# Kernel optimization log

Hardware: AMD Instinct MI355X
Metric: run time of the kernel (lower is better)

The kernel has to match this reference:

```python
import jax, jax.numpy as jnp
import numpy as np

NEG_SLOPE = 0.2  # PyG GATConv default
BN_EPS = 1e-5
NUM_GRAPHS = 128


def _bn(x, g, b, m, v):
    # eval-mode BatchNorm1d with running stats
    return (x - m) * jax.lax.rsqrt(v + BN_EPS) * g + b


def _gat_conv(x, src, dst, mask, W, a_src, a_dst, bias):
    # PyG GATConv: per-head linear, edge logits LeakyReLU(a_src.Wx_j + a_dst.Wx_i),
    # segment-softmax over incoming edges of each dst node, scatter-add messages.
    N = x.shape[0]
    H, C = a_src.shape
    xw = (x @ W).reshape(N, H, C)                       # [N,H,C]
    logit_s = (xw * a_src).sum(-1)                      # [N,H]
    logit_d = (xw * a_dst).sum(-1)                      # [N,H]
    e = jax.nn.leaky_relu(logit_s[src] + logit_d[dst], NEG_SLOPE)  # [E,H]
    e = jnp.where(mask[:, None], e, -1e30)              # edges filtered by edge_weights==1
    m = jax.ops.segment_max(e, dst, num_segments=N)     # [N,H]
    m = jnp.maximum(m, -1e30)                           # guard empty segments
    p = jnp.exp(e - m[dst]) * mask[:, None].astype(e.dtype)
    denom = jax.ops.segment_sum(p, dst, num_segments=N) + 1e-16
    alpha = p / denom[dst]                              # [E,H]
    out = jax.ops.segment_sum(xw[src] * alpha[..., None], dst, num_segments=N)
    return out.reshape(N, H * C) + bias


def setup_inputs() -> dict:
    key = jax.random.key(0)
    ks = jax.random.split(key, 20)
    N, E, F, G, NC = 20000, 320000, 128, NUM_GRAPHS, 10
    E0, E1, H = 256, 512, 2
    C = E1 // H

    def lin(k, fi, fo):
        return jax.random.normal(k, (fi, fo), jnp.float32) / np.float32(np.sqrt(fi))

    def bn(k, n):
        k1, k2, k3, k4 = jax.random.split(k, 4)
        g = 1.0 + 0.1 * jax.random.normal(k1, (n,), jnp.float32)
        b = 0.1 * jax.random.normal(k2, (n,), jnp.float32)
        m = 0.1 * jax.random.normal(k3, (n,), jnp.float32)
        v = 1.0 + 0.5 * jax.random.uniform(k4, (n,), jnp.float32)
        return g, b, m, v

    d = {}
    d['x'] = jax.random.normal(ks[0], (N, F), jnp.float32)
    d['edge_index'] = jax.random.randint(ks[1], (2, E), 0, N, dtype=jnp.int32)
    d['edge_weights'] = jnp.ones((E,), jnp.int32)
    d['batch'] = jnp.sort(jax.random.randint(ks[2], (N,), 0, G, dtype=jnp.int32))
    d['mlp_w1'] = lin(ks[3], F, E0); d['mlp_b1'] = jnp.zeros((E0,), jnp.float32)
    d['bn1_g'], d['bn1_b'], d['bn1_m'], d['bn1_v'] = bn(ks[4], E0)
    d['mlp_w2'] = lin(ks[5], E0, E0); d['mlp_b2'] = jnp.zeros((E0,), jnp.float32)
    d['bn2_g'], d['bn2_b'], d['bn2_m'], d['bn2_v'] = bn(ks[6], E0)
    d['gat0_w'] = lin(ks[7], E0, H * C)
    d['gat0_asrc'] = 0.1 * jax.random.normal(ks[8], (H, C), jnp.float32)
    d['gat0_adst'] = 0.1 * jax.random.normal(ks[9], (H, C), jnp.float32)
    d['gat0_bias'] = jnp.zeros((H * C,), jnp.float32)
    d['gat1_w'] = lin(ks[10], E1, H * C)
    d['gat1_asrc'] = 0.1 * jax.random.normal(ks[11], (H, C), jnp.float32)
    d['gat1_adst'] = 0.1 * jax.random.normal(ks[12], (H, C), jnp.float32)
    d['gat1_bias'] = jnp.zeros((H * C,), jnp.float32)
    d['bn3_g'], d['bn3_b'], d['bn3_m'], d['bn3_v'] = bn(ks[13], E1)
    d['fin_w1'] = lin(ks[14], E1, E1); d['fin_b1'] = jnp.zeros((E1,), jnp.float32)
    d['fin_w2'] = lin(ks[15], E1, NC); d['fin_b2'] = jnp.zeros((NC,), jnp.float32)
    return d


def reference(x, edge_index, edge_weights, batch,
              mlp_w1, mlp_b1, bn1_g, bn1_b, bn1_m, bn1_v,
              mlp_w2, mlp_b2, bn2_g, bn2_b, bn2_m, bn2_v,
              gat0_w, gat0_asrc, gat0_adst, gat0_bias,
              gat1_w, gat1_asrc, gat1_adst, gat1_bias,
              bn3_g, bn3_b, bn3_m, bn3_v,
              fin_w1, fin_b1, fin_w2, fin_b2):
    src, dst = edge_index[0], edge_index[1]
    mask = edge_weights == 1
    # initial MLP (dropout is identity in eval)
    h = jax.nn.relu(_bn(x @ mlp_w1 + mlp_b1, bn1_g, bn1_b, bn1_m, bn1_v))
    h = jax.nn.relu(_bn(h @ mlp_w2 + mlp_b2, bn2_g, bn2_b, bn2_m, bn2_v))
    # GAT layers
    h = _gat_conv(h, src, dst, mask, gat0_w, gat0_asrc, gat0_adst, gat0_bias)
    h = _gat_conv(h, src, dst, mask, gat1_w, gat1_asrc, gat1_adst, gat1_bias)
    # global mean pool over graphs
    sums = jax.ops.segment_sum(h, batch, num_segments=NUM_GRAPHS)
    cnt = jax.ops.segment_sum(jnp.ones((h.shape[0], 1), h.dtype), batch, num_segments=NUM_GRAPHS)
    pooled = sums / jnp.maximum(cnt, 1.0)
    # final head: BN -> ReLU -> Linear -> ReLU -> Linear
    z = jax.nn.relu(_bn(pooled, bn3_g, bn3_b, bn3_m, bn3_v))
    z = jax.nn.relu(z @ fin_w1 + fin_b1)
    return z @ fin_w2 + fin_b2
```

## Files before the change

kernel.cpp:

```cpp
#include <hip/hip_runtime.h>

typedef unsigned short u16;

constexpr int NN = 20000;
constexpr int EE = 320000;
constexpr int FD = 128;
constexpr int C0 = 256;
constexpr int C1 = 512;
constexpr int NG = 128;
constexpr int NC = 10;
constexpr int NBLK = (NN + 255) / 256;
constexpr int HB  = 320;
constexpr int EST = HB * 256;

constexpr size_t OFF_XB   = 0;
constexpr size_t OFF_H1   = OFF_XB  + (size_t)NN * FD * 2;
constexpr size_t OFF_H2   = OFF_H1  + (size_t)NN * C0 * 2;
constexpr size_t OFF_XW   = OFF_H2  + (size_t)NN * C0 * 2;
constexpr size_t OFF_H34  = OFF_XW  + (size_t)NN * C1 * 2;
constexpr size_t OFF_LS   = OFF_H34 + (size_t)NN * C1 * 2;
constexpr size_t OFF_LD   = OFF_LS  + (size_t)NN * 2 * 4;
constexpr size_t OFF_DEG  = OFF_LD  + (size_t)NN * 2 * 4;
constexpr size_t OFF_OFFS = OFF_DEG + (size_t)NN * 4;
constexpr size_t OFF_CUR  = OFF_OFFS + 80016;
constexpr size_t OFF_CSRC = OFF_CUR + (size_t)NN * 4;
constexpr size_t OFF_GCNT = OFF_CSRC + (size_t)EE * 4;
constexpr size_t OFF_GOFF = OFF_GCNT + 512;
constexpr size_t OFF_PART = OFF_GOFF + 768;
constexpr size_t OFF_PTOT = OFF_PART + 512;
constexpr size_t OFF_Z1   = OFF_PTOT + 256;
constexpr size_t OFF_Z2   = OFF_Z1  + (size_t)NG * C1 * 2;
constexpr size_t OFF_ST   = OFF_Z2  + (size_t)NG * C1 * 2;
constexpr size_t OFF_W1T  = OFF_ST  + 8192;
constexpr size_t OFF_W2T  = OFF_W1T + (size_t)FD * C0 * 2;
constexpr size_t OFF_G0T  = OFF_W2T + (size_t)C0 * C0 * 2;
constexpr size_t OFF_G1T  = OFF_G0T + (size_t)C0 * C1 * 2;
constexpr size_t OFF_AUX  = OFF_G1T + (size_t)C1 * C1 * 2;
constexpr size_t OFF_FLAG = OFF_AUX  + 0;
constexpr size_t OFF_A0S  = OFF_AUX  + 256;
constexpr size_t OFF_A0D  = OFF_AUX  + 1280;
constexpr size_t OFF_A1S  = OFF_AUX  + 2304;
constexpr size_t OFF_A1D  = OFF_AUX  + 3328;
constexpr size_t OFF_GB0  = OFF_AUX  + 4352;
constexpr size_t OFF_GB1  = OFF_AUX  + 6400;
constexpr size_t OFF_FB1  = OFF_AUX  + 8448;
constexpr size_t OFF_FB2  = OFF_AUX  + 10496;
constexpr size_t OFF_GMX  = OFF_AUX  + 10752;

__device__ inline float bf2f(u16 u) { return __uint_as_float(((unsigned)u) << 16); }
__device__ inline u16 f2bf(float f) {
    unsigned u = __float_as_uint(f);
    unsigned r = u + 0x7fffu + ((u >> 16) & 1u);
    return (u16)(r >> 16);
}
__device__ inline float ldf(const void* p, long i, unsigned f) {
    return f ? ((const float*)p)[i] : bf2f(((const u16*)p)[i]);
}
__device__ inline unsigned encf(float f) {
    unsigned u = __float_as_uint(f);
    return (u & 0x80000000u) ? ~u : (u | 0x80000000u);
}
__device__ inline float decf(unsigned e) {
    return (e & 0x80000000u) ? __uint_as_float(e ^ 0x80000000u) : __uint_as_float(~e);
}
__device__ inline void unpack8(uint4 r, float* v) {
    v[0] = bf2f((u16)(r.x & 0xffff)); v[1] = bf2f((u16)(r.x >> 16));
    v[2] = bf2f((u16)(r.y & 0xffff)); v[3] = bf2f((u16)(r.y >> 16));
    v[4] = bf2f((u16)(r.z & 0xffff)); v[5] = bf2f((u16)(r.z >> 16));
    v[6] = bf2f((u16)(r.w & 0xffff)); v[7] = bf2f((u16)(r.w >> 16));
}

typedef __bf16 bf16x8_t __attribute__((ext_vector_type(8)));
typedef float  f32x4_t  __attribute__((ext_vector_type(4)));

__device__ __forceinline__ void gl_lds16(const u16* g, u16* l) {
    __builtin_amdgcn_global_load_lds((const __attribute__((address_space(1))) void*)g,
                                     (__attribute__((address_space(3))) void*)l, 16, 0, 0);
}

__global__ void detect_dtype(const u16* __restrict__ x, const u16* __restrict__ w,
                             const u16* __restrict__ fw, unsigned* flag) {
    __shared__ int cnt;
    if (threadIdx.x == 0) cnt = 0;
    __syncthreads();
    int c = 0;
    for (int i = threadIdx.x; i < 4096; i += 256) {
        c += (((x[i]  >> 7) & 0xFF) == 0xFF);
        c += (((w[i]  >> 7) & 0xFF) == 0xFF);
        c += (((fw[i] >> 7) & 0xFF) == 0xFF);
    }
    atomicAdd(&cnt, c);
    __syncthreads();
    if (threadIdx.x == 0) *flag = (cnt >= 2) ? 1u : 0u;
}

__global__ void cvt_x(const unsigned* __restrict__ flag, const void* __restrict__ xin,
                      u16* __restrict__ XB, int* __restrict__ deg, int* __restrict__ gcnt,
                      unsigned* __restrict__ gmxu) {
    int i = blockIdx.x * 256 + threadIdx.x;
    if (i < NN) deg[i] = 0;
    if (i < NG) gcnt[i] = 0;
    if (i < 4)  gmxu[i] = encf(-1e30f);
    if (*flag) {
        float4 v = ((const float4*)xin)[i];
        ushort4 r;
        r.x = f2bf(v.x); r.y = f2bf(v.y); r.z = f2bf(v.z); r.w = f2bf(v.w);
        ((ushort4*)XB)[i] = r;
    } else {
        ((ushort4*)XB)[i] = ((const ushort4*)xin)[i];
    }
}

__global__ void prep_params(const unsigned* __restrict__ flag,
                            const void* g1, const void* b1, const void* m1, const void* v1, const void* lb1,
                            const void* g2, const void* b2, const void* m2, const void* v2, const void* lb2,
                            const void* g3, const void* b3, const void* m3, const void* v3,
                            const void* a0s, const void* a0d, const void* gb0in,
                            const void* a1s, const void* a1d, const void* gb1in,
                            const void* fb1in, const void* fb2in,
                            float* S1, float* T1, float* S2, float* T2, float* S3, float* T3,
                            u16* A0S, u16* A0D, u16* A1S, u16* A1D,
                            float* GB0, float* GB1, float* FB1, float* FB2) {
    unsigned f = *flag;
    int c = threadIdx.x;
    if (c < 256) {
        float s = ldf(g1, c, f) / sqrtf(ldf(v1, c, f) + 1e-5f);
        S1[c] = s; T1[c] = s * (ldf(lb1, c, f) - ldf(m1, c, f)) + ldf(b1, c, f);
        float s2 = ldf(g2, c, f) / sqrtf(ldf(v2, c, f) + 1e-5f);
        S2[c] = s2; T2[c] = s2 * (ldf(lb2, c, f) - ldf(m2, c, f)) + ldf(b2, c, f);
    }
    float s3 = ldf(g3, c, f) / sqrtf(ldf(v3, c, f) + 1e-5f);
    S3[c] = s3; T3[c] = ldf(b3, c, f) - ldf(m3, c, f) * s3;
    A0S[c] = f2bf(ldf(a0s, c, f));
    A0D[c] = f2bf(ldf(a0d, c, f));
    A1S[c] = f2bf(ldf(a1s, c, f));
    A1D[c] = f2bf(ldf(a1d, c, f));
    GB0[c] = ldf(gb0in, c, f);
    GB1[c] = ldf(gb1in, c, f);
    FB1[c] = ldf(fb1in, c, f);
    if (c < NC) FB2[c] = ldf(fb2in, c, f);
}

__global__ void transpose_all(const unsigned* __restrict__ flag,
                              const void* __restrict__ w1, const void* __restrict__ w2,
                              const void* __restrict__ g0, const void* __restrict__ g1,
                              u16* __restrict__ w1T, u16* __restrict__ w2T,
                              u16* __restrict__ g0T, u16* __restrict__ g1T) {
    int b = blockIdx.x;
    const void* B; u16* BT; int K, logN, base;
    if (b < 128)      { B = w1; BT = w1T; K = FD; logN = 8; base = 0; }
    else if (b < 384) { B = w2; BT = w2T; K = C0; logN = 8; base = 128; }
    else if (b < 896) { B = g0; BT = g0T; K = C0; logN = 9; base = 384; }
    else              { B = g1; BT = g1T; K = C1; logN = 9; base = 896; }
    int idx = (b - base) * 256 + threadIdx.x;
    int N = 1 << logN;
    int k = idx >> logN, n = idx & (N - 1);
    u16 v = (*flag) ? f2bf(((const float*)B)[idx]) : ((const u16*)B)[idx];
    BT[(size_t)n * K + k] = v;
}

__global__ __launch_bounds__(256) void hist_k(const int* __restrict__ dst, const int* __restrict__ ew,
                                              const int* __restrict__ batch,
                                              int* __restrict__ deg, int* __restrict__ gcnt) {
    int tid = blockIdx.x * 256 + threadIdx.x;
    int lane = threadIdx.x & 63;
#pragma unroll
    for (int j = 0; j < 4; j++) {
        int e = tid + j * EST;
        if (e < EE && ew[e] == 1) atomicAdd(&deg[dst[e]], 1);
    }
    int n = tid;
    if (n < NN) {
        int g = batch[n];
        int pg = __shfl_up(g, 1);
        bool head = (lane == 0) || (pg != g);
        unsigned long long act = __ballot(1);
        unsigned long long hm  = __ballot(head);
        if (head) {
            unsigned long long above = (lane < 63) ? ((hm >> (lane + 1)) << (lane + 1)) : 0ull;
            int limit = 64 - __builtin_clzll(act);
            int nxt = above ? __builtin_ctzll(above) : limit;
            atomicAdd(&gcnt[g], nxt - lane);
        }
    }
}
__global__ __launch_bounds__(256) void scan_blk(const int* __restrict__ deg, int* __restrict__ off,
                                                int* __restrict__ part) {
    __shared__ int tmp[256];
    int tid = threadIdx.x, i = blockIdx.x * 256 + tid;
    int v = (i < NN) ? deg[i] : 0;
    tmp[tid] = v;
    __syncthreads();
#pragma unroll
    for (int s = 1; s < 256; s <<= 1) {
        int a = (tid >= s) ? tmp[tid - s] : 0;
        __syncthreads();
        if (tid >= s) tmp[tid] += a;
        __syncthreads();
    }
    if (i < NN) off[i] = tmp[tid] - v;
    if (tid == 255) part[blockIdx.x] = tmp[255];
}
__global__ __launch_bounds__(128) void scan_small(int* __restrict__ part, int* __restrict__ ptot,
                                                  const int* __restrict__ gcnt, int* __restrict__ goff) {
    __shared__ int tmp[128];
    int tid = threadIdx.x;
    int v = (tid < NBLK) ? part[tid] : 0;
    tmp[tid] = v;
    __syncthreads();
#pragma unroll
    for (int s = 1; s < 128; s <<= 1) {
        int a = (tid >= s) ? tmp[tid - s] : 0;
        __syncthreads();
        if (tid >= s) tmp[tid] += a;
        __syncthreads();
    }
    if (tid < NBLK) part[tid] = tmp[tid] - v;
    if (tid == 127) *ptot = tmp[127];
    __syncthreads();
    int g = gcnt[tid];
    tmp[tid] = g;
    __syncthreads();
#pragma unroll
    for (int s = 1; s < 128; s <<= 1) {
        int a = (tid >= s) ? tmp[tid - s] : 0;
        __syncthreads();
        if (tid >= s) tmp[tid] += a;
        __syncthreads();
    }
    goff[tid] = tmp[tid] - g;
    if (tid == 127) goff[128] = tmp[127];
}
__global__ __launch_bounds__(256) void scan_add(int* __restrict__ off, const int* __restrict__ part,
                                                const int* __restrict__ ptot, int* __restrict__ cursor) {
    int tid = threadIdx.x, i = blockIdx.x * 256 + tid;
    if (i < NN) {
        int o = off[i] + part[blockIdx.x];
        off[i] = o;
        cursor[i] = o;
    }
    if (i == 0) off[NN] = *ptot;
}
__global__ __launch_bounds__(256) void csr_fill(const int* __restrict__ src, const int* __restrict__ dst,
                                                const int* __restrict__ ew,
                                                int* __restrict__ cursor, int* __restrict__ csrc) {
    int tid = blockIdx.x * 256 + threadIdx.x;
    bool ok[4]; int sv[4]; int p[4];
#pragma unroll
    for (int j = 0; j < 4; j++) {
        int e = tid + j * EST;
        ok[j] = false; sv[j] = 0; p[j] = 0;
        if (e < EE && ew[e] == 1) {
            ok[j] = true;
            sv[j] = src[e];
            p[j] = atomicAdd(&cursor[dst[e]], 1);
        }
    }
#pragma unroll
    for (int j = 0; j < 4; j++) if (ok[j]) csrc[p[j]] = sv[j];
}

template <int EPI>
__global__ __launch_bounds__(256) void gemm_tile(const u16* __restrict__ A, const u16* __restrict__ BT,
                                                 u16* __restrict__ Cm,
                                                 const float* __restrict__ S, const float* __restrict__ T,
                                                 int M, int N, int K) {
    __shared__ u16 As[64 * 32];
    __shared__ u16 Bs[128 * 32];
    const int tid  = threadIdx.x;
    const int wave = tid >> 6;
    const int lane = tid & 63;
    const int quad = lane >> 4;
    const int l16  = lane & 15;
    const int wr0  = (wave >> 1) * 32;
    const int wc0  = (wave & 1) * 64;
    const int row0 = blockIdx.x * 64;
    const int col0 = blockIdx.y * 128;

    const int lr = lane >> 2;
    const int lk = (lane & 3) * 8;
    const u16* gp[3];
    u16* lp[3];
#pragma unroll
    for (int j = 0; j < 3; j++) {
        int t = wave * 3 + j;
        if (t < 4) {
            int rl = t * 16 + lr;
            int gr = row0 + rl; if (gr >= M) gr = M - 1;
            gp[j] = A + (size_t)gr * K + lk;
            lp[j] = As + t * 512 + lane * 8;
        } else {
            int bl = (t - 4) * 16 + lr;
            gp[j] = BT + (size_t)(col0 + bl) * K + lk;
            lp[j] = Bs + (t - 4) * 512 + lane * 8;
        }
    }

    f32x4_t acc[2][4];
#pragma unroll
    for (int r = 0; r < 2; r++)
#pragma unroll
        for (int c = 0; c < 4; c++)
#pragma unroll
            for (int i = 0; i < 4; i++) acc[r][c][i] = 0.f;

    for (int k0 = 0; k0 < K; k0 += 32) {
#pragma unroll
        for (int j = 0; j < 3; j++) gl_lds16(gp[j] + k0, lp[j]);
        __syncthreads();

        bf16x8_t a[2], b[4];
#pragma unroll
        for (int r = 0; r < 2; r++)
            a[r] = *(const bf16x8_t*)(As + (size_t)(wr0 + r * 16 + l16) * 32 + quad * 8);
#pragma unroll
        for (int c = 0; c < 4; c++)
            b[c] = *(const bf16x8_t*)(Bs + (size_t)(wc0 + c * 16 + l16) * 32 + quad * 8);
#pragma unroll
        for (int r = 0; r < 2; r++)
#pragma unroll
            for (int c = 0; c < 4; c++)
                acc[r][c] = __builtin_amdgcn_mfma_f32_16x16x32_bf16(a[r], b[c], acc[r][c], 0, 0, 0);
        __syncthreads();
    }

#pragma unroll
    for (int r = 0; r < 2; r++) {
        int rb = row0 + wr0 + r * 16 + quad * 4;
#pragma unroll
        for (int c = 0; c < 4; c++) {
            int col = col0 + wc0 + c * 16 + l16;
            float sc = (EPI == 1) ? S[col] : 0.f;
            float sh = (EPI == 1) ? T[col] : 0.f;
#pragma unroll
            for (int i = 0; i < 4; i++) {
                int row = rb + i;
                if (row < M) {
                    float v = acc[r][c][i];
                    if (EPI == 1) v = fmaxf(v * sc + sh, 0.f);
                    Cm[(size_t)row * N + col] = f2bf(v);
                }
            }
        }
    }
}

__global__ __launch_bounds__(256) void gat_logits(const u16* __restrict__ xw, const u16* __restrict__ asrc,
                                                  const u16* __restrict__ adst, float* __restrict__ ls,
                                                  float* __restrict__ ld) {
    int n = blockIdx.x * 4 + (threadIdx.x >> 6);
    if (n >= NN) return;
    int lane = threadIdx.x & 63;
    uint4 xv = ((const uint4*)(xw + (size_t)n * C1))[lane];
    uint4 sv = ((const uint4*)asrc)[lane];
    uint4 dv = ((const uint4*)adst)[lane];
    float x[8], a[8], d[8];
    unpack8(xv, x); unpack8(sv, a); unpack8(dv, d);
    float ps = 0.f, pd = 0.f;
#pragma unroll
    for (int j = 0; j < 8; j++) { ps += x[j] * a[j]; pd += x[j] * d[j]; }
#pragma unroll
    for (int m = 16; m >= 1; m >>= 1) { ps += __shfl_xor(ps, m); pd += __shfl_xor(pd, m); }
    if ((lane & 31) == 0) {
        int h = lane >> 5;
        ls[n * 2 + h] = ps;
        ld[n * 2 + h] = pd;
    }
}

__global__ __launch_bounds__(256) void ls_max(const float* __restrict__ ls, unsigned* __restrict__ gmx) {
    int tid = blockIdx.x * 256 + threadIdx.x;
    float m0 = -1e30f, m1 = -1e30f;
    for (int n = tid; n < NN; n += 40 * 256) {
        float2 v = ((const float2*)ls)[n];
        m0 = fmaxf(m0, v.x); m1 = fmaxf(m1, v.y);
    }
#pragma unroll
    for (int o = 32; o >= 1; o >>= 1) {
        m0 = fmaxf(m0, __shfl_xor(m0, o));
        m1 = fmaxf(m1, __shfl_xor(m1, o));
    }
    if ((threadIdx.x & 63) == 0) {
        atomicMax(&gmx[0], encf(m0));
        atomicMax(&gmx[1], encf(m1));
    }
}

__global__ __launch_bounds__(256) void gat_aggregate(const int* __restrict__ off, const int* __restrict__ csrc,
                                                     const float* __restrict__ ls, const float* __restrict__ ld,
                                                     const unsigned* __restrict__ gmx, const u16* __restrict__ xw,
                                                     const float* __restrict__ bias, u16* __restrict__ outh) {
    int n = blockIdx.x * 4 + (threadIdx.x >> 6);
    if (n >= NN) return;
    int lane = threadIdx.x & 63;
    int h = lane >> 5;
    int beg = off[n], end = off[n + 1];
    float ldh = ld[n * 2 + h];
    float gm = decf(gmx[h]) + ldh;
    float mhat = gm > 0.f ? gm : 0.2f * gm;

    float acc[8];
#pragma unroll
    for (int j = 0; j < 8; j++) acc[j] = 0.f;
    float den = 0.f;

    float lsv = 0.f; uint4 row;
    if (beg < end) {
        int s0 = csrc[beg];
        lsv = ls[s0 * 2 + h];
        row = ((const uint4*)(xw + (size_t)s0 * C1))[lane];
    }
    for (int i = beg; i < end; i++) {
        float cls = lsv;
        uint4 crow = row;
        if (i + 1 < end) {
            int s2 = csrc[i + 1];
            lsv = ls[s2 * 2 + h];
            row = ((const uint4*)(xw + (size_t)s2 * C1))[lane];
        }
        float v = cls + ldh;
        v = v > 0.f ? v : 0.2f * v;
        float p = __expf(v - mhat);
        den += p;
        float x[8];
        unpack8(crow, x);
#pragma unroll
        for (int j = 0; j < 8; j++) acc[j] = fmaf(p, x[j], acc[j]);
    }

    float inv = 1.f / fmaxf(den, 1e-30f);
    ushort4 r0, r1;
    int cb = lane * 8;
    float o0 = acc[0] * inv + bias[cb + 0], o1 = acc[1] * inv + bias[cb + 1];
    float o2 = acc[2] * inv + bias[cb + 2], o3 = acc[3] * inv + bias[cb + 3];
    float o4 = acc[4] * inv + bias[cb + 4], o5 = acc[5] * inv + bias[cb + 5];
    float o6 = acc[6] * inv + bias[cb + 6], o7 = acc[7] * inv + bias[cb + 7];
    r0.x = f2bf(o0); r0.y = f2bf(o1); r0.z = f2bf(o2); r0.w = f2bf(o3);
    r1.x = f2bf(o4); r1.y = f2bf(o5); r1.z = f2bf(o6); r1.w = f2bf(o7);
    ushort4* dst4 = (ushort4*)(outh + (size_t)n * C1 + cb);
    dst4[0] = r0; dst4[1] = r1;
}

__global__ __launch_bounds__(512) void pool_bn(const u16* __restrict__ h4, const int* __restrict__ goff,
                                               const float* __restrict__ S3, const float* __restrict__ T3,
                                               u16* __restrict__ z1) {
    int g = blockIdx.x, t = threadIdx.x;
    int b = goff[g], e = goff[g + 1];
    float s = 0.f;
    for (int n = b; n < e; n++) s += bf2f(h4[(size_t)n * C1 + t]);
    float mean = s / fmaxf((float)(e - b), 1.f);
    float v = mean * S3[t] + T3[t];
    z1[(size_t)g * C1 + t] = f2bf(fmaxf(v, 0.f));
}

__global__ __launch_bounds__(512) void head_fc1(const unsigned* __restrict__ flag, const u16* __restrict__ z1,
                                                const void* __restrict__ w1, const float* __restrict__ FB1,
                                                u16* __restrict__ z2) {
    __shared__ float zrow[512];
    int g = blockIdx.x, t = threadIdx.x;
    zrow[t] = bf2f(z1[(size_t)g * 512 + t]);
    __syncthreads();
    float acc = 0.f;
    if (*flag) {
        const float* w = (const float*)w1;
        for (int k = 0; k < 512; k++) acc = fmaf(zrow[k], w[(size_t)k * 512 + t], acc);
    } else {
        const u16* w = (const u16*)w1;
        for (int k = 0; k < 512; k++) acc = fmaf(zrow[k], bf2f(w[(size_t)k * 512 + t]), acc);
    }
    acc += FB1[t];
    z2[(size_t)g * 512 + t] = f2bf(fmaxf(acc, 0.f));
}
__global__ __launch_bounds__(64) void head_fc2(const unsigned* __restrict__ flag, const u16* __restrict__ z2,
                                               const void* __restrict__ w2, const float* __restrict__ FB2,
                                               void* __restrict__ out) {
    int g = blockIdx.x, o = blockIdx.y, lane = threadIdx.x;
    unsigned f = *flag;
    float acc = 0.f;
    if (f) {
        const float* w = (const float*)w2;
        for (int k = lane; k < 512; k += 64) acc += bf2f(z2[(size_t)g * 512 + k]) * w[(size_t)k * NC + o];
    } else {
        const u16* w = (const u16*)w2;
        for (int k = lane; k < 512; k += 64) acc += bf2f(z2[(size_t)g * 512 + k]) * bf2f(w[(size_t)k * NC + o]);
    }
#pragma unroll
    for (int m = 32; m >= 1; m >>= 1) acc += __shfl_xor(acc, m);
    if (lane == 0) {
        float v = acc + FB2[o];
        if (f) ((float*)out)[g * NC + o] = v;
        else   ((u16*)out)[g * NC + o] = f2bf(v);
    }
}

extern "C" void kernel_launch(void* const* d_in, const int* in_sizes, int n_in,
                              void* d_out, int out_size, void* d_ws, size_t ws_size,
                              hipStream_t stream) {
    (void)in_sizes; (void)n_in; (void)out_size; (void)ws_size;

    const void* x      = d_in[0];
    const int* ei      = (const int*)d_in[1];
    const int* src     = ei;
    const int* dst     = ei + EE;
    const int* ew      = (const int*)d_in[2];
    const int* batch   = (const int*)d_in[3];
    const void* mlp_w1 = d_in[4];
    const void* mlp_b1 = d_in[5];
    const void *bn1g = d_in[6], *bn1b = d_in[7], *bn1m = d_in[8], *bn1v = d_in[9];
    const void* mlp_w2 = d_in[10];
    const void* mlp_b2 = d_in[11];
    const void *bn2g = d_in[12], *bn2b = d_in[13], *bn2m = d_in[14], *bn2v = d_in[15];
    const void* g0w    = d_in[16];
    const void* g0as   = d_in[17];
    const void* g0ad   = d_in[18];
    const void* g0bias = d_in[19];
    const void* g1w    = d_in[20];
    const void* g1as   = d_in[21];
    const void* g1ad   = d_in[22];
    const void* g1bias = d_in[23];
    const void *bn3g = d_in[24], *bn3b = d_in[25], *bn3m = d_in[26], *bn3v = d_in[27];
    const void* fin_w1 = d_in[28];
    const void* fin_b1 = d_in[29];
    const void* fin_w2 = d_in[30];
    const void* fin_b2 = d_in[31];

    char* ws = (char*)d_ws;
    u16*  XB   = (u16*)(ws + OFF_XB);
    u16*  h1   = (u16*)(ws + OFF_H1);
    u16*  h2   = (u16*)(ws + OFF_H2);
    u16*  xw   = (u16*)(ws + OFF_XW);
    u16*  h34  = (u16*)(ws + OFF_H34);
    float* ls  = (float*)(ws + OFF_LS);
    float* ld  = (float*)(ws + OFF_LD);
    int*  deg  = (int*)(ws + OFF_DEG);
    int*  off  = (int*)(ws + OFF_OFFS);
    int*  cur  = (int*)(ws + OFF_CUR);
    int*  csrc = (int*)(ws + OFF_CSRC);
    int*  gcnt = (int*)(ws + OFF_GCNT);
    int*  goff = (int*)(ws + OFF_GOFF);
    int*  part = (int*)(ws + OFF_PART);
    int*  ptot = (int*)(ws + OFF_PTOT);
    u16*  z1   = (u16*)(ws + OFF_Z1);
    u16*  z2   = (u16*)(ws + OFF_Z2);
    float* S1 = (float*)(ws + OFF_ST);
    float* T1 = S1 + 256;
    float* S2 = T1 + 256;
    float* T2 = S2 + 256;
    float* S3 = T2 + 256;
    float* T3 = S3 + 512;
    u16* w1T = (u16*)(ws + OFF_W1T);
    u16* w2T = (u16*)(ws + OFF_W2T);
    u16* g0T = (u16*)(ws + OFF_G0T);
    u16* g1T = (u16*)(ws + OFF_G1T);
    unsigned* flag = (unsigned*)(ws + OFF_FLAG);
    u16* A0S = (u16*)(ws + OFF_A0S);
    u16* A0D = (u16*)(ws + OFF_A0D);
    u16* A1S = (u16*)(ws + OFF_A1S);
    u16* A1D = (u16*)(ws + OFF_A1D);
    float* GB0 = (float*)(ws + OFF_GB0);
    float* GB1 = (float*)(ws + OFF_GB1);
    float* FB1 = (float*)(ws + OFF_FB1);
    float* FB2 = (float*)(ws + OFF_FB2);
    unsigned* GMXU = (unsigned*)(ws + OFF_GMX);

    detect_dtype<<<1, 256, 0, stream>>>((const u16*)x, (const u16*)mlp_w1, (const u16*)fin_w1, flag);
    cvt_x<<<(NN * FD / 4) / 256, 256, 0, stream>>>(flag, x, XB, deg, gcnt, GMXU);
    prep_params<<<1, 512, 0, stream>>>(flag,
                                       bn1g, bn1b, bn1m, bn1v, mlp_b1,
                                       bn2g, bn2b, bn2m, bn2v, mlp_b2,
                                       bn3g, bn3b, bn3m, bn3v,
                                       g0as, g0ad, g0bias, g1as, g1ad, g1bias,
                                       fin_b1, fin_b2,
                                       S1, T1, S2, T2, S3, T3,
                                       A0S, A0D, A1S, A1D, GB0, GB1, FB1, FB2);
    transpose_all<<<1920, 256, 0, stream>>>(flag, mlp_w1, mlp_w2, g0w, g1w, w1T, w2T, g0T, g1T);

    hist_k<<<HB, 256, 0, stream>>>(dst, ew, batch, deg, gcnt);
    scan_blk<<<NBLK, 256, 0, stream>>>(deg, off, part);
    scan_small<<<1, 128, 0, stream>>>(part, ptot, gcnt, goff);
    scan_add<<<NBLK, 256, 0, stream>>>(off, part, ptot, cur);
    csr_fill<<<HB, 256, 0, stream>>>(src, dst, ew, cur, csrc);

    gemm_tile<1><<<dim3(313, 2), 256, 0, stream>>>(XB, w1T, h1, S1, T1, NN, C0, FD);
    gemm_tile<1><<<dim3(313, 2), 256, 0, stream>>>(h1, w2T, h2, S2, T2, NN, C0, C0);

    gemm_tile<0><<<dim3(313, 4), 256, 0, stream>>>(h2, g0T, xw, nullptr, nullptr, NN, C1, C0);
    gat_logits<<<NN / 4, 256, 0, stream>>>(xw, A0S, A0D, ls, ld);
    ls_max<<<40, 256, 0, stream>>>(ls, GMXU);
    gat_aggregate<<<NN / 4, 256, 0, stream>>>(off, csrc, ls, ld, GMXU, xw, GB0, h34);

    gemm_tile<0><<<dim3(313, 4), 256, 0, stream>>>(h34, g1T, xw, nullptr, nullptr, NN, C1, C1);
    gat_logits<<<NN / 4, 256, 0, stream>>>(xw, A1S, A1D, ls, ld);
    ls_max<<<40, 256, 0, stream>>>(ls, GMXU + 2);
    gat_aggregate<<<NN / 4, 256, 0, stream>>>(off, csrc, ls, ld, GMXU + 2, xw, GB1, h34);

    pool_bn<<<NG, 512, 0, stream>>>(h34, goff, S3, T3, z1);
    head_fc1<<<NG, 512, 0, stream>>>(flag, z1, fin_w1, FB1, z2);
    head_fc2<<<dim3(NG, NC), 64, 0, stream>>>(flag, z2, fin_w2, FB2, d_out);
}
```

Measured before the change: 441.0 us.

## Split GAT aggregation into per-head feature slices with edge-parallel half-waves

Replaces the one-wave-per-node GAT aggregation with eight blocks per node group, each covering a 64-feature slice of one head. Each wave splits into two halves that process alternating incoming edges, each lane holding two features; the halves' partial sums are combined with a cross-lane shuffle before the output is written. The aim is more parallelism and shorter serial dependency chains over each node's edges. The cost is that edge indices, logits and exponentials are recomputed in every slice, and each lane's gather shrinks to 4-byte loads with no prefetch of the next edge.

```diff
diff --git a/kernel.cpp b/kernel.cpp
--- a/kernel.cpp
+++ b/kernel.cpp
@@ -386,59 +386,49 @@
     }
 }
 
-__global__ __launch_bounds__(256) void gat_aggregate(const int* __restrict__ off, const int* __restrict__ csrc,
+__global__ __launch_bounds__(256) void gat_agg_slice(const int* __restrict__ off, const int* __restrict__ csrc,
                                                      const float* __restrict__ ls, const float* __restrict__ ld,
                                                      const unsigned* __restrict__ gmx, const u16* __restrict__ xw,
                                                      const float* __restrict__ bias, u16* __restrict__ outh) {
-    int n = blockIdx.x * 4 + (threadIdx.x >> 6);
+    int blk = blockIdx.x;
+    int s   = blk & 7;
+    int nb  = blk >> 3;
+    int n   = nb * 4 + (threadIdx.x >> 6);
     if (n >= NN) return;
     int lane = threadIdx.x & 63;
-    int h = lane >> 5;
+    int half = lane >> 5;
+    int h    = s >> 2;
+    int fabs = (s & 3) * 64 + h * 256 + (lane & 31) * 2;
+
     int beg = off[n], end = off[n + 1];
     float ldh = ld[n * 2 + h];
     float gm = decf(gmx[h]) + ldh;
     float mhat = gm > 0.f ? gm : 0.2f * gm;
 
-    float acc[8];
-#pragma unroll
-    for (int j = 0; j < 8; j++) acc[j] = 0.f;
-    float den = 0.f;
-
-    float lsv = 0.f; uint4 row;
-    if (beg < end) {
-        int s0 = csrc[beg];
-        lsv = ls[s0 * 2 + h];
-        row = ((const uint4*)(xw + (size_t)s0 * C1))[lane];
-    }
-    for (int i = beg; i < end; i++) {
-        float cls = lsv;
-        uint4 crow = row;
-        if (i + 1 < end) {
-            int s2 = csrc[i + 1];
-            lsv = ls[s2 * 2 + h];
-            row = ((const uint4*)(xw + (size_t)s2 * C1))[lane];
+    float a0 = 0.f, a1 = 0.f, den = 0.f;
+    for (int i = beg; i < end; i += 2) {
+        int e = i + half;
+        float p = 0.f; unsigned rv = 0;
+        if (e < end) {
+            int srcn = csrc[e];
+            float v = ls[srcn * 2 + h] + ldh;
+            v = v > 0.f ? v : 0.2f * v;
+            p = __expf(v - mhat);
+            rv = *(const unsigned*)(xw + (size_t)srcn * C1 + fabs);
         }
-        float v = cls + ldh;
-        v = v > 0.f ? v : 0.2f * v;
-        float p = __expf(v - mhat);
         den += p;
-        float x[8];
-        unpack8(crow, x);
-#pragma unroll
-        for (int j = 0; j < 8; j++) acc[j] = fmaf(p, x[j], acc[j]);
-    }
-
-    float inv = 1.f / fmaxf(den, 1e-30f);
-    ushort4 r0, r1;
-    int cb = lane * 8;
-    float o0 = acc[0] * inv + bias[cb + 0], o1 = acc[1] * inv + bias[cb + 1];
-    float o2 = acc[2] * inv + bias[cb + 2], o3 = acc[3] * inv + bias[cb + 3];
-    float o4 = acc[4] * inv + bias[cb + 4], o5 = acc[5] * inv + bias[cb + 5];
-    float o6 = acc[6] * inv + bias[cb + 6], o7 = acc[7] * inv + bias[cb + 7];
-    r0.x = f2bf(o0); r0.y = f2bf(o1); r0.z = f2bf(o2); r0.w = f2bf(o3);
-    r1.x = f2bf(o4); r1.y = f2bf(o5); r1.z = f2bf(o6); r1.w = f2bf(o7);
-    ushort4* dst4 = (ushort4*)(outh + (size_t)n * C1 + cb);
-    dst4[0] = r0; dst4[1] = r1;
+        a0 = fmaf(p, bf2f((u16)(rv & 0xffff)), a0);
+        a1 = fmaf(p, bf2f((u16)(rv >> 16)), a1);
+    }
+    a0  += __shfl_xor(a0, 32);
+    a1  += __shfl_xor(a1, 32);
+    den += __shfl_xor(den, 32);
+    if (half == 0) {
+        float inv = 1.f / fmaxf(den, 1e-30f);
+        unsigned o = ((unsigned)f2bf(a1 * inv + bias[fabs + 1]) << 16) |
+                     (unsigned)f2bf(a0 * inv + bias[fabs]);
+        *(unsigned*)(outh + (size_t)n * C1 + fabs) = o;
+    }
 }
 
 __global__ __launch_bounds__(512) void pool_bn(const u16* __restrict__ h4, const int* __restrict__ goff,
@@ -587,12 +577,12 @@
     gemm_tile<0><<<dim3(313, 4), 256, 0, stream>>>(h2, g0T, xw, nullptr, nullptr, NN, C1, C0);
     gat_logits<<<NN / 4, 256, 0, stream>>>(xw, A0S, A0D, ls, ld);
     ls_max<<<40, 256, 0, stream>>>(ls, GMXU);
-    gat_aggregate<<<NN / 4, 256, 0, stream>>>(off, csrc, ls, ld, GMXU, xw, GB0, h34);
+    gat_agg_slice<<<8 * ((NN + 3) / 4), 256, 0, stream>>>(off, csrc, ls, ld, GMXU, xw, GB0, h34);
 
     gemm_tile<0><<<dim3(313, 4), 256, 0, stream>>>(h34, g1T, xw, nullptr, nullptr, NN, C1, C1);
     gat_logits<<<NN / 4, 256, 0, stream>>>(xw, A1S, A1D, ls, ld);
     ls_max<<<40, 256, 0, stream>>>(ls, GMXU + 2);
-    gat_aggregate<<<NN / 4, 256, 0, stream>>>(off, csrc, ls, ld, GMXU + 2, xw, GB1, h34);
+    gat_agg_slice<<<8 * ((NN + 3) / 4), 256, 0, stream>>>(off, csrc, ls, ld, GMXU + 2, xw, GB1, h34);
 
     pool_bn<<<NG, 512, 0, stream>>>(h34, goff, S3, T3, z1);
     head_fc1<<<NG, 512, 0, stream>>>(flag, z1, fin_w1, FB1, z2);
```

New measurement: 553.5 us. 1.26x slower.
